# Kernel tuning notes

Measured on AMD Instinct MI355X. Metric: run time of the kernel, lower is better.

The kernel has to match this reference:

```python
import jax, jax.numpy as jnp
import numpy as np

MODEL_DIM = 1024
NUM_HEADS = 16
HEAD_DIM = MODEL_DIM // NUM_HEADS


def setup_inputs() -> dict:
    key = jax.random.key(0)
    ks = jax.random.split(key, 5)
    B, T, D = 4, 2048, MODEL_DIM
    scale = 1.0 / np.sqrt(D)
    x = jax.random.normal(ks[0], (B, T, D), dtype=jnp.float32)
    W_qkv = jax.random.normal(ks[1], (D, 3 * D), dtype=jnp.float32) * scale
    b_qkv = jnp.zeros((3 * D,), dtype=jnp.float32)
    W_out = jax.random.normal(ks[2], (D, D), dtype=jnp.float32) * scale
    b_out = jnp.zeros((D,), dtype=jnp.float32)
    return {"x": x, "W_qkv": W_qkv, "b_qkv": b_qkv, "W_out": W_out, "b_out": b_out}


def reference(x, W_qkv, b_qkv, W_out, b_out):
    B, T, D = x.shape
    H, Hd = NUM_HEADS, HEAD_DIM
    qkv = x @ W_qkv + b_qkv                      # [B,T,3D]
    q, k, v = jnp.split(qkv, 3, axis=-1)
    # [B,T,D] -> [B,H,T,Hd]
    q = q.reshape(B, T, H, Hd).transpose(0, 2, 1, 3)
    k = k.reshape(B, T, H, Hd).transpose(0, 2, 1, 3)
    v = v.reshape(B, T, H, Hd).transpose(0, 2, 1, 3)
    scores = jnp.einsum('bhqd,bhkd->bhqk', q, k) * (1.0 / np.sqrt(Hd))
    causal = jnp.tril(jnp.ones((T, T), dtype=bool))
    scores = jnp.where(causal[None, None], scores, -jnp.inf)
    attn = jax.nn.softmax(scores, axis=-1)
    out = jnp.einsum('bhqk,bhkd->bhqd', attn, v)  # [B,H,T,Hd]
    out = out.transpose(0, 2, 1, 3).reshape(B, T, D)
    return out @ W_out + b_out
```

## Files before the change

kernel.cpp:

```cpp
#include <hip/hip_runtime.h>
#include <stdint.h>

#define T_SEQ   2048
#define DMODEL  1024
#define NHEADS  16
#define HDIM    64
#define BATCH   4
#define MROWS   (BATCH * T_SEQ)
#define QSCALE  0.18033688011112042f
#define DEFER_THR 6.0f

typedef __attribute__((ext_vector_type(4))) short bf16x4;
typedef __attribute__((ext_vector_type(8))) short bf16x8;
typedef __attribute__((ext_vector_type(4))) float f32x4;

__device__ __forceinline__ unsigned short f2b(float f) {
    union { float f; unsigned int i; } x;
    x.f = f;
    unsigned int r = x.i + 0x7FFFu + ((x.i >> 16) & 1u);
    return (unsigned short)(r >> 16);
}

__device__ __forceinline__ float fexp2(float x) {
#if __has_builtin(__builtin_amdgcn_exp2f)
    return __builtin_amdgcn_exp2f(x);
#else
    return __expf(x * 0.6931471805599453f);
#endif
}

__device__ __forceinline__ unsigned int pack2(float a, float b) {
#if __has_builtin(__builtin_amdgcn_cvt_pk_bf16_f32)
    auto r = __builtin_amdgcn_cvt_pk_bf16_f32(a, b);
    unsigned int u;
    __builtin_memcpy(&u, &r, 4);
    return u;
#else
    return ((unsigned int)f2b(a)) | (((unsigned int)f2b(b)) << 16);
#endif
}

__device__ __forceinline__ float max16(const f32x4 s[4]) {
    const float a = fmaxf(fmaxf(s[0][0], s[0][1]), fmaxf(s[0][2], s[0][3]));
    const float b = fmaxf(fmaxf(s[1][0], s[1][1]), fmaxf(s[1][2], s[1][3]));
    const float c = fmaxf(fmaxf(s[2][0], s[2][1]), fmaxf(s[2][2], s[2][3]));
    const float d = fmaxf(fmaxf(s[3][0], s[3][1]), fmaxf(s[3][2], s[3][3]));
    return fmaxf(fmaxf(a, b), fmaxf(c, d));
}

__device__ __forceinline__ void online_softmax(
    const f32x4 sg[4], float& m_, float& l_, f32x4 o_[4], bf16x4 pf_[4])
{
    float mc = max16(sg);
    mc = fmaxf(mc, __shfl_xor(mc, 16));
    mc = fmaxf(mc, __shfl_xor(mc, 32));
    if (__any(mc > m_ + DEFER_THR)) {
        const float mn    = fmaxf(m_, mc);
        const float alpha = fexp2(m_ - mn);
        l_ *= alpha;
        #pragma unroll
        for (int dt = 0; dt < 4; dt++)
            #pragma unroll
            for (int r = 0; r < 4; r++) o_[dt][r] *= alpha;
        m_ = mn;
    }
    float ps = 0.f;
    #pragma unroll
    for (int s = 0; s < 4; s++) {
        const float p0 = fexp2(sg[s][0] - m_);
        const float p1 = fexp2(sg[s][1] - m_);
        const float p2 = fexp2(sg[s][2] - m_);
        const float p3 = fexp2(sg[s][3] - m_);
        ps += (p0 + p1) + (p2 + p3);
        uint2 u;
        u.x = pack2(p0, p1);
        u.y = pack2(p2, p3);
        pf_[s] = *(bf16x4*)&u;
    }
    ps += __shfl_xor(ps, 16);
    ps += __shfl_xor(ps, 32);
    l_ += ps;
}

__device__ __forceinline__ void gl_lds16(const unsigned short* g, unsigned short* l) {
    __builtin_amdgcn_global_load_lds(
        (const __attribute__((address_space(1))) void*)g,
        (__attribute__((address_space(3))) void*)l,
        16, 0, 0);
}

__global__ __launch_bounds__(256) void cvt_bf16(
    const float* __restrict__ in, unsigned short* __restrict__ out, int n)
{
    const int i = (blockIdx.x * 256 + threadIdx.x) * 4;
    if (i + 3 < n) {
        const float4 v = *(const float4*)(in + i);
        ushort4 o;
        o.x = f2b(v.x); o.y = f2b(v.y); o.z = f2b(v.z); o.w = f2b(v.w);
        *(ushort4*)(out + i) = o;
    }
}

__global__ __launch_bounds__(256) void cvt_tr(
    const float* __restrict__ W, unsigned short* __restrict__ WT, int K, int N)
{
    __shared__ unsigned short s[32][33];
    const int n0 = blockIdx.x * 32, k0 = blockIdx.y * 32;
    const int tx = threadIdx.x & 31, ty = threadIdx.x >> 5;
    #pragma unroll
    for (int i = 0; i < 4; i++)
        s[ty + 8 * i][tx] = f2b(W[(size_t)(k0 + ty + 8 * i) * N + n0 + tx]);
    __syncthreads();
    #pragma unroll
    for (int i = 0; i < 4; i++)
        WT[(size_t)(n0 + ty + 8 * i) * K + k0 + tx] = s[tx][ty + 8 * i];
}

template<int KD, int NCOLS, int MODE>
__global__ __launch_bounds__(256) void gemm_mfma(
    const unsigned short* __restrict__ A,
    const unsigned short* __restrict__ BT,
    const float* __restrict__ bias,
    unsigned short* __restrict__ Oq,
    unsigned short* __restrict__ Ok,
    unsigned short* __restrict__ Ov,
    float* __restrict__ Of)
{
    __shared__ __align__(16) unsigned short aS[128 * 64];
    __shared__ __align__(16) unsigned short bS[128 * 64];

    const int tid  = threadIdx.x;
    const int lane = tid & 63;
    const int wave = tid >> 6;
    const int row  = lane & 15;
    const int quad = lane >> 4;
    const int wm   = wave >> 1;
    const int wn   = wave & 1;

    constexpr int NT  = NCOLS / 128;
    constexpr int MT8 = (MROWS / 128) / 8;
    const int orig = blockIdx.x + blockIdx.y * NT;
    const int xcd  = orig & 7;
    const int pos  = orig >> 3;
    const int nt   = pos >> 3;
    const int mtl  = pos & (MT8 - 1);
    const int m0   = (xcd * MT8 + mtl) * 128;
    const int n0   = nt * 128;

    const int srow = lane >> 3;
    const int c8   = lane & 7;
    const int csw  = c8 ^ srow;

    const unsigned short* aG = A  + (size_t)(m0 + wave * 8 + srow) * KD + csw * 8;
    const unsigned short* bG = BT + (size_t)(n0 + wave * 8 + srow) * KD + csw * 8;

    f32x4 acc[4][4];
    const f32x4 z = {0.f, 0.f, 0.f, 0.f};
    #pragma unroll
    for (int i = 0; i < 4; i++)
        #pragma unroll
        for (int j = 0; j < 4; j++) acc[i][j] = z;

    for (int k0 = 0; k0 < KD; k0 += 64) {
        __syncthreads();
        #pragma unroll
        for (int c = 0; c < 4; c++) {
            gl_lds16(aG + c * (32 * KD), &aS[c * 2048 + wave * 512]);
            gl_lds16(bG + c * (32 * KD), &bS[c * 2048 + wave * 512]);
        }
        __syncthreads();
        aG += 64;
        bG += 64;

        #pragma unroll
        for (int ks = 0; ks < 2; ks++) {
            bf16x8 af[4], bf[4];
            const int cp = ((ks * 4 + quad) ^ (row & 7)) * 8;
            #pragma unroll
            for (int t = 0; t < 4; t++) {
                af[t] = *(const bf16x8*)(aS + (wm * 64 + t * 16 + row) * 64 + cp);
                bf[t] = *(const bf16x8*)(bS + (wn * 64 + t * 16 + row) * 64 + cp);
            }
            #pragma unroll
            for (int i = 0; i < 4; i++)
                #pragma unroll
                for (int j = 0; j < 4; j++)
                    acc[i][j] = __builtin_amdgcn_mfma_f32_16x16x32_bf16(af[i], bf[j], acc[i][j], 0, 0, 0);
        }
    }

    if (MODE == 0) {
        #pragma unroll
        for (int j = 0; j < 4; j++) {
            const int n  = n0 + wn * 64 + j * 16 + row;
            const float bi = bias[n];
            const int which = n >> 10;
            const int rem   = n & 1023;
            const int h     = rem >> 6;
            const int d     = rem & 63;
            #pragma unroll
            for (int i = 0; i < 4; i++) {
                const int mbase = m0 + wm * 64 + i * 16 + quad * 4;
                #pragma unroll
                for (int r = 0; r < 4; r++) {
                    const int m = mbase + r;
                    const int b = m >> 11;
                    const int t = m & 2047;
                    const int bh = b * NHEADS + h;
                    const float v = acc[i][j][r] + bi;
                    if (which == 0) {
                        Oq[((size_t)bh * T_SEQ + t) * HDIM + d] = f2b(v * QSCALE);
                    } else if (which == 1) {
                        Ok[((size_t)bh * T_SEQ + t) * HDIM + d] = f2b(v);
                    } else {
                        Ov[((size_t)bh * HDIM + d) * T_SEQ + t] = f2b(v);
                    }
                }
            }
        }
    } else {
        #pragma unroll
        for (int j = 0; j < 4; j++) {
            const int n  = n0 + wn * 64 + j * 16 + row;
            const float bi = bias[n];
            #pragma unroll
            for (int i = 0; i < 4; i++) {
                const int mbase = m0 + wm * 64 + i * 16 + quad * 4;
                #pragma unroll
                for (int r = 0; r < 4; r++)
                    Of[(size_t)(mbase + r) * NCOLS + n] = acc[i][j][r] + bi;
            }
        }
    }
}

__global__ __launch_bounds__(512, 4) void attn_mfma(
    const unsigned short* __restrict__ Q,
    const unsigned short* __restrict__ K,
    const unsigned short* __restrict__ VT,
    unsigned short* __restrict__ Out)
{
    __shared__ __align__(16) unsigned short kS[2][64 * 72];
    __shared__ __align__(16) unsigned short vS[2][64 * 72];

    const int tid  = threadIdx.x;
    const int lane = tid & 63;
    const int wave = tid >> 6;
    const int row  = lane & 15;
    const int quad = lane >> 4;

    const int bh = blockIdx.x;
    const int b  = bh >> 4;
    const int h  = bh & 15;
    const int i  = 15 - (int)blockIdx.y;
    const int q0 = 128 * i + 16 * wave;
    const int kend = 128 * i + 128;

    const size_t qkbase = (size_t)bh * T_SEQ * HDIM;
    const size_t vtbase = (size_t)bh * HDIM * T_SEQ;

    const int krow0 = tid >> 3;
    const int c0    = tid & 7;
    const int lds0  = krow0 * 72 + c0 * 8;
    const int flat0 = tid * 8;

    const unsigned short* qp = Q + qkbase + (size_t)(q0 + row) * HDIM + quad * 8;
    const bf16x8 qf0 = *(const bf16x8*)qp;
    const bf16x8 qf1 = *(const bf16x8*)(qp + 32);

    const f32x4 z = {0.f, 0.f, 0.f, 0.f};
    f32x4 o[4] = {z, z, z, z};
    float m_ = -1e30f, l_ = 0.f;

    uint4 pk0 = *(const uint4*)(K  + qkbase + flat0);
    uint4 pv0 = *(const uint4*)(VT + vtbase + (size_t)krow0 * T_SEQ + c0 * 8);

    int buf = 0;
    for (int kb = 0; kb < kend; kb += 64) {
        *(uint4*)&kS[buf][lds0] = pk0;
        *(uint4*)&vS[buf][lds0] = pv0;
        __syncthreads();

        if (kb + 64 < kend) {
            const int kn = kb + 64;
            pk0 = *(const uint4*)(K  + qkbase + (size_t)kn * HDIM + flat0);
            pv0 = *(const uint4*)(VT + vtbase + (size_t)krow0 * T_SEQ + kn + c0 * 8);
        }

        const bool act = (kb <= q0);

        if (act) {
            f32x4 sg[4];
            bf16x4 pf[4];
            #pragma unroll
            for (int s = 0; s < 4; s++) {
                const int kbs = kb + s * 16;
                if (kbs <= q0) {
                    const unsigned short* kp = &kS[buf][(s * 16 + row) * 72 + quad * 8];
                    const bf16x8 kf0 = *(const bf16x8*)kp;
                    const bf16x8 kf1 = *(const bf16x8*)(kp + 32);
                    f32x4 t = z;
                    t = __builtin_amdgcn_mfma_f32_16x16x32_bf16(kf0, qf0, t, 0, 0, 0);
                    t = __builtin_amdgcn_mfma_f32_16x16x32_bf16(kf1, qf1, t, 0, 0, 0);
                    if (kbs == q0) {
                        #pragma unroll
                        for (int r = 0; r < 4; r++)
                            if (quad * 4 + r > row) t[r] = -1e30f;
                    }
                    sg[s] = t;
                } else {
                    #pragma unroll
                    for (int r = 0; r < 4; r++) sg[s][r] = -1e30f;
                }
            }
            online_softmax(sg, m_, l_, o, pf);

            #pragma unroll
            for (int s = 0; s < 4; s++) {
                const int kbs = kb + s * 16;
                if (kbs <= q0) {
                    #pragma unroll
                    for (int dt = 0; dt < 4; dt++) {
                        const bf16x4 vf = *(const bf16x4*)&vS[buf][
                            (dt * 16 + row) * 72 + (s * 2 + (quad >> 1)) * 8 + (quad & 1) * 4];
                        o[dt] = __builtin_amdgcn_mfma_f32_16x16x16bf16_1k(vf, pf[s], o[dt], 0, 0, 0);
                    }
                }
            }
        }

        buf ^= 1;
    }

    {
        const float rl = 1.f / l_;
        unsigned short* op = Out + ((size_t)(b * T_SEQ + q0 + row)) * DMODEL + h * HDIM + quad * 4;
        #pragma unroll
        for (int dt = 0; dt < 4; dt++) {
            uint2 u;
            u.x = pack2(o[dt][0] * rl, o[dt][1] * rl);
            u.y = pack2(o[dt][2] * rl, o[dt][3] * rl);
            *(uint2*)(op + dt * 16) = u;
        }
    }
}

extern "C" void kernel_launch(void* const* d_in, const int* in_sizes, int n_in,
                              void* d_out, int out_size, void* d_ws, size_t ws_size,
                              hipStream_t stream)
{
    const float* x    = (const float*)d_in[0];
    const float* Wqkv = (const float*)d_in[1];
    const float* bqkv = (const float*)d_in[2];
    const float* Wout = (const float*)d_in[3];
    const float* bout = (const float*)d_in[4];
    float* out = (float*)d_out;

    char* ws = (char*)d_ws;
    unsigned short* xb    = (unsigned short*)(ws + (size_t)0  * 1024 * 1024);
    unsigned short* WqkvT = (unsigned short*)(ws + (size_t)16 * 1024 * 1024);
    unsigned short* WoutT = (unsigned short*)(ws + (size_t)22 * 1024 * 1024);
    unsigned short* Qb    = (unsigned short*)(ws + (size_t)24 * 1024 * 1024);
    unsigned short* Kb    = (unsigned short*)(ws + (size_t)40 * 1024 * 1024);
    unsigned short* Vt    = (unsigned short*)(ws + (size_t)56 * 1024 * 1024);
    unsigned short* Ab    = (unsigned short*)(ws + (size_t)72 * 1024 * 1024);

    cvt_bf16<<<dim3(MROWS * DMODEL / 1024), 256, 0, stream>>>(x, xb, MROWS * DMODEL);
    cvt_tr<<<dim3(3 * DMODEL / 32, DMODEL / 32), 256, 0, stream>>>(Wqkv, WqkvT, DMODEL, 3 * DMODEL);
    cvt_tr<<<dim3(DMODEL / 32, DMODEL / 32), 256, 0, stream>>>(Wout, WoutT, DMODEL, DMODEL);

    gemm_mfma<DMODEL, 3 * DMODEL, 0><<<dim3(3 * DMODEL / 128, MROWS / 128), 256, 0, stream>>>(
        xb, WqkvT, bqkv, Qb, Kb, Vt, nullptr);

    attn_mfma<<<dim3(BATCH * NHEADS, 16), 512, 0, stream>>>(Qb, Kb, Vt, Ab);

    gemm_mfma<DMODEL, DMODEL, 1><<<dim3(DMODEL / 128, MROWS / 128), 256, 0, stream>>>(
        Ab, WoutT, bout, nullptr, nullptr, nullptr, out);
}
```

Baseline: 267.3 us.

## Process two 16-row query tiles per wave in attention with 256-thread blocks

The attention kernel now runs 4 waves of 256 threads instead of 8, and each wave handles two 16-row query tiles (A and B), keeping separate softmax state for each. K and V fragments read from LDS are reused across both tiles, which halves LDS reads per unit of work. Each thread now loads two K and two V chunks per tile. This raises register pressure and gives fewer waves per block, which may reduce latency hiding.

```diff
diff --git a/kernel.cpp b/kernel.cpp
--- a/kernel.cpp
+++ b/kernel.cpp
@@ -234,7 +234,7 @@
     }
 }
 
-__global__ __launch_bounds__(512, 4) void attn_mfma(
+__global__ __launch_bounds__(256, 4) void attn_mfma(
     const unsigned short* __restrict__ Q,
     const unsigned short* __restrict__ K,
     const unsigned short* __restrict__ VT,
@@ -253,7 +253,8 @@
     const int b  = bh >> 4;
     const int h  = bh & 15;
     const int i  = 15 - (int)blockIdx.y;
-    const int q0 = 128 * i + 16 * wave;
+    const int q0a = 128 * i + 32 * wave;
+    const int q0b = q0a + 16;
     const int kend = 128 * i + 128;
 
     const size_t qkbase = (size_t)bh * T_SEQ * HDIM;
@@ -262,68 +263,96 @@
     const int krow0 = tid >> 3;
     const int c0    = tid & 7;
     const int lds0  = krow0 * 72 + c0 * 8;
+    const int lds1  = (krow0 + 32) * 72 + c0 * 8;
     const int flat0 = tid * 8;
 
-    const unsigned short* qp = Q + qkbase + (size_t)(q0 + row) * HDIM + quad * 8;
-    const bf16x8 qf0 = *(const bf16x8*)qp;
-    const bf16x8 qf1 = *(const bf16x8*)(qp + 32);
+    const unsigned short* qpa = Q + qkbase + (size_t)(q0a + row) * HDIM + quad * 8;
+    const bf16x8 qa0 = *(const bf16x8*)qpa;
+    const bf16x8 qa1 = *(const bf16x8*)(qpa + 32);
+    const unsigned short* qpb = Q + qkbase + (size_t)(q0b + row) * HDIM + quad * 8;
+    const bf16x8 qb0 = *(const bf16x8*)qpb;
+    const bf16x8 qb1 = *(const bf16x8*)(qpb + 32);
 
     const f32x4 z = {0.f, 0.f, 0.f, 0.f};
-    f32x4 o[4] = {z, z, z, z};
-    float m_ = -1e30f, l_ = 0.f;
+    f32x4 oA[4] = {z, z, z, z};
+    f32x4 oB[4] = {z, z, z, z};
+    float mA = -1e30f, lA = 0.f, mB = -1e30f, lB = 0.f;
 
     uint4 pk0 = *(const uint4*)(K  + qkbase + flat0);
-    uint4 pv0 = *(const uint4*)(VT + vtbase + (size_t)krow0 * T_SEQ + c0 * 8);
+    uint4 pk1 = *(const uint4*)(K  + qkbase + flat0 + 2048);
+    uint4 pv0 = *(const uint4*)(VT + vtbase + (size_t)krow0        * T_SEQ + c0 * 8);
+    uint4 pv1 = *(const uint4*)(VT + vtbase + (size_t)(krow0 + 32) * T_SEQ + c0 * 8);
 
     int buf = 0;
     for (int kb = 0; kb < kend; kb += 64) {
         *(uint4*)&kS[buf][lds0] = pk0;
+        *(uint4*)&kS[buf][lds1] = pk1;
         *(uint4*)&vS[buf][lds0] = pv0;
+        *(uint4*)&vS[buf][lds1] = pv1;
         __syncthreads();
 
         if (kb + 64 < kend) {
             const int kn = kb + 64;
             pk0 = *(const uint4*)(K  + qkbase + (size_t)kn * HDIM + flat0);
-            pv0 = *(const uint4*)(VT + vtbase + (size_t)krow0 * T_SEQ + kn + c0 * 8);
-        }
-
-        const bool act = (kb <= q0);
-
-        if (act) {
-            f32x4 sg[4];
-            bf16x4 pf[4];
+            pk1 = *(const uint4*)(K  + qkbase + (size_t)kn * HDIM + flat0 + 2048);
+            pv0 = *(const uint4*)(VT + vtbase + (size_t)krow0        * T_SEQ + kn + c0 * 8);
+            pv1 = *(const uint4*)(VT + vtbase + (size_t)(krow0 + 32) * T_SEQ + kn + c0 * 8);
+        }
+
+        if (kb <= q0b) {
+            f32x4 sgA[4], sgB[4];
+            bf16x4 pfA[4], pfB[4];
             #pragma unroll
             for (int s = 0; s < 4; s++) {
                 const int kbs = kb + s * 16;
-                if (kbs <= q0) {
+                if (kbs <= q0b) {
                     const unsigned short* kp = &kS[buf][(s * 16 + row) * 72 + quad * 8];
                     const bf16x8 kf0 = *(const bf16x8*)kp;
                     const bf16x8 kf1 = *(const bf16x8*)(kp + 32);
                     f32x4 t = z;
-                    t = __builtin_amdgcn_mfma_f32_16x16x32_bf16(kf0, qf0, t, 0, 0, 0);
-                    t = __builtin_amdgcn_mfma_f32_16x16x32_bf16(kf1, qf1, t, 0, 0, 0);
-                    if (kbs == q0) {
+                    t = __builtin_amdgcn_mfma_f32_16x16x32_bf16(kf0, qb0, t, 0, 0, 0);
+                    t = __builtin_amdgcn_mfma_f32_16x16x32_bf16(kf1, qb1, t, 0, 0, 0);
+                    if (kbs == q0b) {
                         #pragma unroll
                         for (int r = 0; r < 4; r++)
                             if (quad * 4 + r > row) t[r] = -1e30f;
                     }
-                    sg[s] = t;
+                    sgB[s] = t;
+                    if (kbs <= q0a) {
+                        f32x4 u = z;
+                        u = __builtin_amdgcn_mfma_f32_16x16x32_bf16(kf0, qa0, u, 0, 0, 0);
+                        u = __builtin_amdgcn_mfma_f32_16x16x32_bf16(kf1, qa1, u, 0, 0, 0);
+                        if (kbs == q0a) {
+                            #pragma unroll
+                            for (int r = 0; r < 4; r++)
+                                if (quad * 4 + r > row) u[r] = -1e30f;
+                        }
+                        sgA[s] = u;
+                    } else {
+                        #pragma unroll
+                        for (int r = 0; r < 4; r++) sgA[s][r] = -1e30f;
+                    }
                 } else {
                     #pragma unroll
-                    for (int r = 0; r < 4; r++) sg[s][r] = -1e30f;
+                    for (int r = 0; r < 4; r++) { sgA[s][r] = -1e30f; sgB[s][r] = -1e30f; }
                 }
             }
-            online_softmax(sg, m_, l_, o, pf);
+            online_softmax(sgB, mB, lB, oB, pfB);
+            if (kb <= q0a)
+                online_softmax(sgA, mA, lA, oA, pfA);
 
             #pragma unroll
             for (int s = 0; s < 4; s++) {
                 const int kbs = kb + s * 16;
-                if (kbs <= q0) {
+                if (kbs <= q0b) {
+                    const bool doA = (kbs <= q0a);
                     #pragma unroll
                     for (int dt = 0; dt < 4; dt++) {
                         const bf16x4 vf = *(const bf16x4*)&vS[buf][
                             (dt * 16 + row) * 72 + (s * 2 + (quad >> 1)) * 8 + (quad & 1) * 4];
-                        o[dt] = __builtin_amdgcn_mfma_f32_16x16x16bf16_1k(vf, pf[s], o[dt], 0, 0, 0);
+                        oB[dt] = __builtin_amdgcn_mfma_f32_16x16x16bf16_1k(vf, pfB[s], oB[dt], 0, 0, 0);
+                        if (doA)
+                            oA[dt] = __builtin_amdgcn_mfma_f32_16x16x16bf16_1k(vf, pfA[s], oA[dt], 0, 0, 0);
                     }
                 }
             }
@@ -333,13 +362,24 @@
     }
 
     {
-        const float rl = 1.f / l_;
-        unsigned short* op = Out + ((size_t)(b * T_SEQ + q0 + row)) * DMODEL + h * HDIM + quad * 4;
+        const float rl = 1.f / lB;
+        unsigned short* op = Out + ((size_t)(b * T_SEQ + q0b + row)) * DMODEL + h * HDIM + quad * 4;
         #pragma unroll
         for (int dt = 0; dt < 4; dt++) {
             uint2 u;
-            u.x = pack2(o[dt][0] * rl, o[dt][1] * rl);
-            u.y = pack2(o[dt][2] * rl, o[dt][3] * rl);
+            u.x = pack2(oB[dt][0] * rl, oB[dt][1] * rl);
+            u.y = pack2(oB[dt][2] * rl, oB[dt][3] * rl);
+            *(uint2*)(op + dt * 16) = u;
+        }
+    }
+    {
+        const float rl = 1.f / lA;
+        unsigned short* op = Out + ((size_t)(b * T_SEQ + q0a + row)) * DMODEL + h * HDIM + quad * 4;
+        #pragma unroll
+        for (int dt = 0; dt < 4; dt++) {
+            uint2 u;
+            u.x = pack2(oA[dt][0] * rl, oA[dt][1] * rl);
+            u.y = pack2(oA[dt][2] * rl, oA[dt][3] * rl);
             *(uint2*)(op + dt * 16) = u;
         }
     }
@@ -372,7 +412,7 @@
     gemm_mfma<DMODEL, 3 * DMODEL, 0><<<dim3(3 * DMODEL / 128, MROWS / 128), 256, 0, stream>>>(
         xb, WqkvT, bqkv, Qb, Kb, Vt, nullptr);
 
-    attn_mfma<<<dim3(BATCH * NHEADS, 16), 512, 0, stream>>>(Qb, Kb, Vt, Ab);
+    attn_mfma<<<dim3(BATCH * NHEADS, 16), 256, 0, stream>>>(Qb, Kb, Vt, Ab);
 
     gemm_mfma<DMODEL, DMODEL, 1><<<dim3(DMODEL / 128, MROWS / 128), 256, 0, stream>>>(
         Ab, WoutT, bout, nullptr, nullptr, nullptr, out);
```

Measured after the change: 318.9 us. 1.19x slower.
